# Optimization experiments

Hardware: AMD Instinct MI355X
Metric: run time of the kernel (lower is better)

Reference implementation:

```python
import jax, jax.numpy as jnp
import numpy as np

K_NEIGHBORS = 8

def _cdist(x, y):
    x2 = jnp.sum(x * x, axis=-1)[:, None]
    y2 = jnp.sum(y * y, axis=-1)[None, :]
    d2 = x2 + y2 - 2.0 * (x @ y.T)
    return jnp.sqrt(jnp.maximum(d2, 0.0))

def setup_inputs() -> dict:
    key = jax.random.key(0)
    ks = jax.random.split(key, 16)
    B, C, H, W = 8, 384, 64, 64
    s = lambda fan: 1.0 / np.sqrt(fan)
    inp = {
        'fea': jax.random.normal(ks[0], (B, C, H, W), dtype=jnp.float32),
        # GCNConv weights (applied as x @ W) and post-aggregation biases
        'W1': jax.random.normal(ks[1], (C, C), jnp.float32) * s(C),
        'b1': jnp.zeros((C,), jnp.float32),
        'W2': jax.random.normal(ks[2], (C, C), jnp.float32) * s(C),
        'b2': jnp.zeros((C,), jnp.float32),
        'W3': jax.random.normal(ks[3], (C, C), jnp.float32) * s(C),
        'b3': jnp.zeros((C,), jnp.float32),
        # uncertainty MLP: C -> C/2 -> C/4 -> 1
        'U1': jax.random.normal(ks[4], (C, C // 2), jnp.float32) * s(C),
        'ub1': jnp.zeros((C // 2,), jnp.float32),
        'U2': jax.random.normal(ks[5], (C // 2, C // 4), jnp.float32) * s(C // 2),
        'ub2': jnp.zeros((C // 4,), jnp.float32),
        'U3': jax.random.normal(ks[6], (C // 4, 1), jnp.float32) * s(C // 4),
        'ub3': jnp.zeros((1,), jnp.float32),
    }
    return inp

def _build_graph(fea, k):
    B, C, H, W = fea.shape
    N = H * W
    gy, gx = jnp.meshgrid(jnp.arange(H), jnp.arange(W), indexing='ij')
    coord = jnp.stack([gy, gx], axis=-1).astype(jnp.float32).reshape(N, 2)
    fea_mean = fea.reshape(B, C, N).transpose(0, 2, 1).mean(0)  # [N, C]
    spatial_dist = _cdist(coord, coord)
    feature_dist = _cdist(fea_mean, fea_mean)
    combined = 0.7 * spatial_dist + 0.3 * feature_dist
    _, topk_idx = jax.lax.top_k(-combined, k)  # smallest-k per row
    src = jnp.repeat(jnp.arange(N), k)         # edge_index[0]
    dst = topk_idx.reshape(-1)                 # edge_index[1]
    return src, dst, N

def _gcn_conv(x, W, b, src, dst, N):
    # PyG GCNConv with symmetric normalization; self-loops are guaranteed
    # by construction (diag of combined dist is 0, strictly minimal), so
    # add_remaining_self_loops is a no-op.
    xw = x @ W                                              # [B, N, C]
    deg = jnp.zeros((N,), x.dtype).at[dst].add(1.0)
    dinv = jax.lax.rsqrt(deg)
    norm = dinv[src] * dinv[dst]                            # [E]
    msgs = xw[:, src, :] * norm[None, :, None]              # [B, E, C]
    out = jnp.zeros_like(xw).at[:, dst, :].add(msgs)
    return out + b

def reference(fea, W1, b1, W2, b2, W3, b3, U1, ub1, U2, ub2, U3, ub3):
    B, C, H, W = fea.shape
    src, dst, N = _build_graph(fea, K_NEIGHBORS)
    x = fea.reshape(B, C, N).transpose(0, 2, 1)             # [B, N, C]
    x = x + jax.nn.relu(_gcn_conv(x, W1, b1, src, dst, N))
    x = x + jax.nn.relu(_gcn_conv(x, W2, b2, src, dst, N))
    x = x + jax.nn.relu(_gcn_conv(x, W3, b3, src, dst, N))
    h = jax.nn.gelu(x @ U1 + ub1)
    h = jax.nn.gelu(h @ U2 + ub2)
    unc = jax.nn.sigmoid(h @ U3 + ub3)                      # [B, N, 1]
    unc = unc.reshape(B, 1, H, W)
    return fea * (1.0 + unc)
```

## Files before the change

kernel.cpp:

```cpp
#include <hip/hip_runtime.h>
#include <hip/hip_bf16.h>
#include <math.h>

#define N_NODES 4096
#define C_DIM   384
#define B_DIM   8
#define K_NB    8
#define E_TOT   (N_NODES * K_NB)
#define M_ROWS  (B_DIM * N_NODES)
#define NCHUNK  4
#define SROW    40

typedef unsigned long long u64;
typedef unsigned short u16;
typedef __attribute__((ext_vector_type(8))) short bf16x8;
typedef __attribute__((ext_vector_type(4))) float f32x4;
#define KEY_INF 0xFFFFFFFFFFFFFFFFull

__device__ __forceinline__ u16 f2bf(float f) {
  unsigned u = __float_as_uint(f);
  u += 0x7FFFu + ((u >> 16) & 1u);
  return (u16)(u >> 16);
}
__device__ __forceinline__ float bf2f(u16 h) {
  return __uint_as_float((unsigned)h << 16);
}
__device__ __forceinline__ f32x4 mfma16(bf16x8 a, bf16x8 b, f32x4 c) {
  return __builtin_amdgcn_mfma_f32_16x16x32_bf16(a, b, c, 0, 0, 0);
}
__device__ __forceinline__ void gl_lds16(const u16* gp, u16* lp) {
  __builtin_amdgcn_global_load_lds(
      (const __attribute__((address_space(1))) unsigned int*)gp,
      (__attribute__((address_space(3))) unsigned int*)lp, 16, 0, 0);
}
__device__ __forceinline__ int xcd_swz(int bid, int nwg) {
  return (bid & 7) * (nwg >> 3) + (bid >> 3);
}

__device__ __forceinline__ void ce(u64& a, u64& b) {
  u64 lo = a < b ? a : b;
  u64 hi = a < b ? b : a;
  a = lo; b = hi;
}
__device__ __forceinline__ void ins8(u64 key, u64 (&r)[8]) {
  if (key < r[7]) {
    #pragma unroll
    for (int i = 0; i < 8; i++) {
      u64 lo = key < r[i] ? key : r[i];
      u64 hi = key < r[i] ? r[i] : key;
      r[i] = lo; key = hi;
    }
  }
}
__device__ __forceinline__ void merge8(u64 (&r)[8], const u64 (&o)[8]) {
  u64 c[8];
  #pragma unroll
  for (int i = 0; i < 8; i++) c[i] = r[i] < o[7 - i] ? r[i] : o[7 - i];
  ce(c[0], c[4]); ce(c[1], c[5]); ce(c[2], c[6]); ce(c[3], c[7]);
  ce(c[0], c[2]); ce(c[1], c[3]); ce(c[4], c[6]); ce(c[5], c[7]);
  ce(c[0], c[1]); ce(c[2], c[3]); ce(c[4], c[5]); ce(c[6], c[7]);
  #pragma unroll
  for (int i = 0; i < 8; i++) r[i] = c[i];
}

__global__ __launch_bounds__(256) void k_prep_w(
    const float* __restrict__ W1, const float* __restrict__ W2,
    const float* __restrict__ W3, const float* __restrict__ U1,
    const float* __restrict__ U2,
    u16* __restrict__ Wt1, u16* __restrict__ Wt2, u16* __restrict__ Wt3,
    u16* __restrict__ U1t, u16* __restrict__ U2t) {
  int idx = blockIdx.x * 256 + threadIdx.x;
  if (idx < 147456) {
    int n = idx / 384, k = idx % 384;
    Wt1[idx] = f2bf(W1[k * 384 + n]);
  } else if (idx < 294912) {
    int i = idx - 147456; int n = i / 384, k = i % 384;
    Wt2[i] = f2bf(W2[k * 384 + n]);
  } else if (idx < 442368) {
    int i = idx - 294912; int n = i / 384, k = i % 384;
    Wt3[i] = f2bf(W3[k * 384 + n]);
  } else if (idx < 516096) {
    int i = idx - 442368; int n = i / 384, k = i % 384;
    U1t[i] = f2bf(U1[k * 192 + n]);
  } else if (idx < 534528) {
    int i = idx - 516096; int n = i / 192, k = i % 192;
    U2t[i] = f2bf(U2[k * 96 + n]);
  }
}

__global__ __launch_bounds__(256) void k_transpose_mean(
    const float* __restrict__ fea, u16* __restrict__ Xb,
    u16* __restrict__ fh, u16* __restrict__ fl) {
  __shared__ float tb[32][132];
  __shared__ float ac[32][132];
  int n0 = blockIdx.x * 128, c0 = blockIdx.y * 32;
  int tx = threadIdx.x, ty = threadIdx.y;
  int flat = ty * 32 + tx;
  int g = flat & 3;
  int r2 = flat >> 2;
  for (int i = ty; i < 32; i += 8) {
    #pragma unroll
    for (int e = 0; e < 4; e++) ac[i][tx * 4 + e] = 0.0f;
  }
  __syncthreads();
  for (int b = 0; b < B_DIM; b++) {
    for (int i = ty; i < 32; i += 8) {
      float4 v = *(const float4*)(fea +
          ((size_t)b * C_DIM + (c0 + i)) * N_NODES + n0 + tx * 4);
      *(float4*)&tb[i][tx * 4] = v;
      ac[i][tx * 4 + 0] += v.x;
      ac[i][tx * 4 + 1] += v.y;
      ac[i][tx * 4 + 2] += v.z;
      ac[i][tx * 4 + 3] += v.w;
    }
    __syncthreads();
    #pragma unroll
    for (int half = 0; half < 2; half++) {
      int r = r2 + 64 * half;
      bf16x8 v;
      #pragma unroll
      for (int cc = 0; cc < 8; cc++) v[cc] = (short)f2bf(tb[g * 8 + cc][r]);
      *(bf16x8*)&Xb[((size_t)b * N_NODES + n0 + r) * C_DIM + c0 + g * 8] = v;
    }
    __syncthreads();
  }
  #pragma unroll
  for (int half = 0; half < 2; half++) {
    int r = r2 + 64 * half;
    bf16x8 vh, vl;
    #pragma unroll
    for (int cc = 0; cc < 8; cc++) {
      float m = ac[g * 8 + cc][r] * 0.125f;
      u16 h = f2bf(m);
      vh[cc] = (short)h;
      vl[cc] = (short)f2bf(m - bf2f(h));
    }
    size_t o = (size_t)(n0 + r) * C_DIM + c0 + g * 8;
    *(bf16x8*)&fh[o] = vh;
    *(bf16x8*)&fl[o] = vl;
  }
}

__global__ __launch_bounds__(64) void k_x2(const u16* __restrict__ fh,
                                           const u16* __restrict__ fl,
                                           float* __restrict__ x2) {
  int n = blockIdx.x;
  int lane = threadIdx.x;
  const u16* rh = fh + (size_t)n * C_DIM;
  const u16* rl = fl + (size_t)n * C_DIM;
  float s = 0.0f;
  for (int c = lane; c < C_DIM; c += 64) {
    float v = bf2f(rh[c]) + bf2f(rl[c]);
    s += v * v;
  }
  for (int d = 32; d > 0; d >>= 1) s += __shfl_down(s, d);
  if (lane == 0) x2[n] = s;
}

__global__ __launch_bounds__(256) void k_dist_win(
    const u16* __restrict__ fh, const u16* __restrict__ fl,
    const float* __restrict__ x2, u64* __restrict__ pk,
    int* __restrict__ deg, int* __restrict__ cnt) {
  __shared__ u16 WH[400 * SROW];
  __shared__ u16 WL[400 * SROW];
  int t = threadIdx.x;
  int lane = t & 63, w = t >> 6;
  int p = blockIdx.x;
  int py = p >> 4, px = p & 15;
  int iy0 = py * 4, ix0 = px * 4;
  int l15 = lane & 15;
  int kb = (lane >> 4) * 8;

  if (p < 16) { deg[p * 256 + t] = 0; cnt[p * 256 + t] = 0; }

  int t0 = (w == 0) ? 0 : 7 + (w - 1) * 6;
  int nt = w ? 6 : 7;

  int jj[7]; float x2j[7]; int jy_[7], jx_[7];
  #pragma unroll
  for (int tt = 0; tt < 7; tt++) {
    int s = (t0 + tt) * 16 + l15;
    int sy = s / 20, sx = s - sy * 20;
    int jy = iy0 - 8 + sy, jx = ix0 - 8 + sx;
    bool v = (tt < nt) && ((unsigned)jy < 64u) && ((unsigned)jx < 64u);
    jj[tt] = v ? (jy * 64 + jx) : -1;
    jy_[tt] = jy; jx_[tt] = jx;
    x2j[tt] = v ? x2[jy * 64 + jx] : 0.0f;
  }
  int pr = 168 + (l15 >> 2) * 20 + (l15 & 3);

  int seg = t & 3;
  int rb = t >> 2;

  f32x4 acc[7];
  #pragma unroll
  for (int tt = 0; tt < 7; tt++) acc[tt] = (f32x4){0.f, 0.f, 0.f, 0.f};

  for (int kc = 0; kc < 12; kc++) {
    int k0 = kc * 32;
    __syncthreads();
    #pragma unroll
    for (int it = 0; it < 7; it++) {
      int r = rb + 64 * it;
      if (r < 400) {
        int sy = r / 20, sx = r - sy * 20;
        int jy = iy0 - 8 + sy, jx = ix0 - 8 + sx;
        int j = (((unsigned)jy < 64u) && ((unsigned)jx < 64u)) ? jy * 64 + jx : 0;
        size_t src = (size_t)j * C_DIM + k0 + seg * 8;
        *(bf16x8*)&WH[r * SROW + seg * 8] = *(const bf16x8*)(fh + src);
        *(bf16x8*)&WL[r * SROW + seg * 8] = *(const bf16x8*)(fl + src);
      }
    }
    __syncthreads();
    bf16x8 aH = *(const bf16x8*)&WH[pr * SROW + kb];
    bf16x8 aL = *(const bf16x8*)&WL[pr * SROW + kb];
    #pragma unroll
    for (int tt = 0; tt < 7; tt++) {
      int row = (t0 + tt) * 16 + l15;
      bf16x8 bH = *(const bf16x8*)&WH[row * SROW + kb];
      bf16x8 bL = *(const bf16x8*)&WL[row * SROW + kb];
      acc[tt] = mfma16(aH, bH, acc[tt]);
      acc[tt] = mfma16(aL, bH, acc[tt]);
      acc[tt] = mfma16(aH, bL, acc[tt]);
    }
  }

  #pragma unroll
  for (int r = 0; r < 4; r++) {
    int r16 = ((lane >> 4) << 2) + r;
    int iy = iy0 + (r16 >> 2), ix = ix0 + (r16 & 3);
    int i = iy * 64 + ix;
    float x2i = x2[i];
    u64 top[8];
    #pragma unroll
    for (int q = 0; q < 8; q++) top[q] = KEY_INF;
    #pragma unroll
    for (int tt = 0; tt < 7; tt++) {
      float d2 = x2i + x2j[tt] - 2.0f * acc[tt][r];
      float fd = sqrtf(fmaxf(d2, 0.0f));
      float dy = (float)(iy - jy_[tt]), dx = (float)(ix - jx_[tt]);
      float sd = sqrtf(dy * dy + dx * dx);
      float comb = 0.7f * sd + 0.3f * fd;
      u64 key = (jj[tt] >= 0)
                    ? (((u64)__float_as_uint(comb) << 12) | (u64)jj[tt])
                    : KEY_INF;
      ins8(key, top);
    }
    #pragma unroll
    for (int d = 1; d < 16; d <<= 1) {
      u64 o[8];
      #pragma unroll
      for (int q = 0; q < 8; q++) o[q] = __shfl_xor(top[q], d);
      merge8(top, o);
    }
    if (l15 == 0) {
      #pragma unroll
      for (int q = 0; q < 8; q++)
        pk[((size_t)w * N_NODES + i) * 8 + q] = top[q];
    }
  }
}

__global__ __launch_bounds__(256) void k_topk_merge_fb(
    const u64* __restrict__ pk, const u16* __restrict__ fh,
    const u16* __restrict__ fl, const float* __restrict__ x2,
    int* __restrict__ tk, int* __restrict__ deg) {
  __shared__ int fl_list[256];
  __shared__ int fl_cnt;
  int t = threadIdx.x;
  if (t == 0) fl_cnt = 0;
  __syncthreads();
  int n = blockIdx.x * 256 + t;
  {
    u64 r[8];
    #pragma unroll
    for (int q = 0; q < 8; q++) r[q] = KEY_INF;
    for (int c = 0; c < NCHUNK; c++) {
      const u64* lst = pk + ((size_t)c * N_NODES + n) * 8;
      #pragma unroll
      for (int q = 0; q < 8; q++) {
        u64 key = lst[q];
        if (key >= r[7]) break;
        ins8(key, r);
      }
    }
    float c8 = __uint_as_float((unsigned)(r[7] >> 12));
    if (c8 > 6.28f) {
      int pos = atomicAdd(&fl_cnt, 1);
      fl_list[pos] = n;
    } else {
      #pragma unroll
      for (int o = 0; o < 8; o++) {
        int idx = (int)(r[o] & 0xFFF);
        tk[n * 8 + o] = idx;
        atomicAdd(&deg[idx], 1);
      }
    }
  }
  __syncthreads();
  int nf = fl_cnt;
  int w = t >> 6, lane = t & 63;
  for (int fi = w; fi < nf; fi += 4) {
    int nn = fl_list[fi];
    u64 top[8];
    #pragma unroll
    for (int q = 0; q < 8; q++) top[q] = KEY_INF;
    float x2i = x2[nn];
    int iy = nn >> 6, ix = nn & 63;
    const u16* rh = fh + (size_t)nn * C_DIM;
    const u16* rl = fl + (size_t)nn * C_DIM;
    for (int jb = 0; jb < N_NODES; jb += 64) {
      int j = jb + lane;
      const u16* ch = fh + (size_t)j * C_DIM;
      const u16* cl = fl + (size_t)j * C_DIM;
      float dot = 0.0f;
      for (int k2 = 0; k2 < C_DIM; k2++)
        dot += (bf2f(rh[k2]) + bf2f(rl[k2])) * (bf2f(ch[k2]) + bf2f(cl[k2]));
      float d2 = x2i + x2[j] - 2.0f * dot;
      float fd = sqrtf(fmaxf(d2, 0.0f));
      float dy = (float)(iy - (j >> 6)), dx = (float)(ix - (j & 63));
      float sd = sqrtf(dy * dy + dx * dx);
      float comb = 0.7f * sd + 0.3f * fd;
      ins8(((u64)__float_as_uint(comb) << 12) | (u64)j, top);
    }
    #pragma unroll
    for (int d = 1; d < 64; d <<= 1) {
      u64 o[8];
      #pragma unroll
      for (int q = 0; q < 8; q++) o[q] = __shfl_xor(top[q], d);
      merge8(top, o);
    }
    if (lane == 0) {
      #pragma unroll
      for (int q = 0; q < 8; q++) {
        int idx = (int)(top[q] & 0xFFF);
        tk[nn * 8 + q] = idx;
        atomicAdd(&deg[idx], 1);
      }
    }
  }
}

__global__ __launch_bounds__(256) void k_scan(const int* __restrict__ deg,
                                              int* __restrict__ offs,
                                              float* __restrict__ dinv) {
  __shared__ int ps[256];
  int t = threadIdx.x;
  int base = t * 16;
  int loc[16]; int s = 0;
  for (int i = 0; i < 16; i++) { int d = deg[base + i]; loc[i] = s; s += d; }
  ps[t] = s;
  __syncthreads();
  for (int d = 1; d < 256; d <<= 1) {
    int add = (t >= d) ? ps[t - d] : 0;
    __syncthreads();
    ps[t] += add;
    __syncthreads();
  }
  int cbase = (t == 0) ? 0 : ps[t - 1];
  for (int i = 0; i < 16; i++) offs[base + i] = cbase + loc[i];
  if (t == 255) offs[N_NODES] = ps[255];
  for (int i = 0; i < 16; i++)
    dinv[base + i] = 1.0f / sqrtf((float)deg[base + i]);
}

__global__ __launch_bounds__(256) void k_fill(const int* __restrict__ tk,
                                              const int* __restrict__ offs,
                                              int* __restrict__ cnt,
                                              int* __restrict__ insrc) {
  int e = blockIdx.x * 256 + threadIdx.x;
  if (e >= E_TOT) return;
  int i = e >> 3;
  int n = tk[e];
  int pos = offs[n] + atomicAdd(&cnt[n], 1);
  insrc[pos] = i;
}

__global__ __launch_bounds__(256) void k_sort(const int* __restrict__ offs,
                                              int* __restrict__ insrc) {
  int n = blockIdx.x * 256 + threadIdx.x;
  if (n >= N_NODES) return;
  int beg = offs[n], end = offs[n + 1];
  for (int a = beg + 1; a < end; a++) {
    int v = insrc[a]; int p = a;
    while (p > beg && insrc[p - 1] > v) { insrc[p] = insrc[p - 1]; p--; }
    insrc[p] = v;
  }
}

__device__ __forceinline__ float gelu_f(float x) {
  const float k0 = 0.7978845608028654f;
  float x3 = x * x * x;
  return 0.5f * x * (1.0f + tanhf(k0 * (x + 0.044715f * x3)));
}

template <int EPI>
__global__ __launch_bounds__(256) void k_gemm_lds(
    const u16* __restrict__ A, const u16* __restrict__ Bt,
    const float* __restrict__ bias, u16* __restrict__ Cout,
    int M, int N, int K, int nnt) {
  __shared__ u16 As[2 * 128 * 32];
  __shared__ u16 Bs[2 * 128 * 32];
  const int BO = 128 * 32;
  int wg = xcd_swz(blockIdx.x, gridDim.x);
  int mt = wg / nnt, ntile = wg - mt * nnt;
  int m0 = mt * 128;
  int n0 = ntile * 128;
  int t = threadIdx.x, lane = t & 63, w = t >> 6;
  int l15 = lane & 15;
  int kg = lane >> 4;
  int wr = (w >> 1) * 64, wc = (w & 1) * 64;

  int srow = w * 32 + (lane >> 2);
  int scol = (lane & 3) * 8;
  const u16* gA0 = A + (size_t)(m0 + srow) * K + scol;
  const u16* gA1 = A + (size_t)(m0 + srow + 16) * K + scol;
  int br0 = n0 + srow;      br0 = (br0 < N) ? br0 : 0;
  int br1 = n0 + srow + 16; br1 = (br1 < N) ? br1 : 0;
  const u16* gB0 = Bt + (size_t)br0 * K + scol;
  const u16* gB1 = Bt + (size_t)br1 * K + scol;
  int lo0 = (w * 32) * 32;
  int lo1 = (w * 32 + 16) * 32;

  f32x4 acc[4][4];
  #pragma unroll
  for (int s = 0; s < 4; s++)
    #pragma unroll
    for (int nt = 0; nt < 4; nt++) acc[s][nt] = (f32x4){0.f, 0.f, 0.f, 0.f};

  gl_lds16(gA0, &As[lo0]);
  gl_lds16(gA1, &As[lo1]);
  gl_lds16(gB0, &Bs[lo0]);
  gl_lds16(gB1, &Bs[lo1]);
  __syncthreads();

  int NT = K / 32;
  for (int kt = 0; kt < NT; kt++) {
    int cur = (kt & 1) * BO;
    if (kt + 1 < NT) {
      int nb = ((kt + 1) & 1) * BO;
      int ko = (kt + 1) * 32;
      gl_lds16(gA0 + ko, &As[nb + lo0]);
      gl_lds16(gA1 + ko, &As[nb + lo1]);
      gl_lds16(gB0 + ko, &Bs[nb + lo0]);
      gl_lds16(gB1 + ko, &Bs[nb + lo1]);
    }
    bf16x8 a[4], b[4];
    #pragma unroll
    for (int s = 0; s < 4; s++)
      a[s] = *(const bf16x8*)&As[cur + (wr + s * 16 + l15) * 32 + kg * 8];
    #pragma unroll
    for (int nt = 0; nt < 4; nt++)
      b[nt] = *(const bf16x8*)&Bs[cur + (wc + nt * 16 + l15) * 32 + kg * 8];
    #pragma unroll
    for (int s = 0; s < 4; s++)
      #pragma unroll
      for (int nt = 0; nt < 4; nt++)
        acc[s][nt] = mfma16(a[s], b[nt], acc[s][nt]);
    if (kt + 1 < NT) __syncthreads();
  }

  #pragma unroll
  for (int s = 0; s < 4; s++) {
    int rbase = m0 + wr + s * 16 + ((lane >> 4) << 2);
    #pragma unroll
    for (int nt = 0; nt < 4; nt++) {
      int n = n0 + wc + nt * 16 + l15;
      if (n >= N) continue;
      float bb = (EPI == 1) ? bias[n] : 0.0f;
      #pragma unroll
      for (int r = 0; r < 4; r++) {
        int m = rbase + r;
        float v = acc[s][nt][r];
        if (EPI == 1) { v += bb; v = gelu_f(v); }
        Cout[(size_t)m * N + n] = f2bf(v);
      }
    }
  }
}

__global__ __launch_bounds__(256) void k_mlp2(
    const u16* __restrict__ A, const u16* __restrict__ Bt,
    const float* __restrict__ ub2, const float* __restrict__ U3,
    const float* __restrict__ ub3, float* __restrict__ unc) {
  const int K = 192;
  int t = threadIdx.x, lane = t & 63, w = t >> 6;
  int m0 = blockIdx.x * 128 + w * 32;
  int l15 = lane & 15;
  int kb = (lane >> 4) * 8;

  f32x4 acc[2][6];
  #pragma unroll
  for (int s = 0; s < 2; s++)
    #pragma unroll
    for (int nt = 0; nt < 6; nt++) acc[s][nt] = (f32x4){0.f, 0.f, 0.f, 0.f};

  const u16* ap = A + (size_t)(m0 + l15) * K + kb;
  const u16* bp[6];
  #pragma unroll
  for (int nt = 0; nt < 6; nt++)
    bp[nt] = Bt + (size_t)(nt * 16 + l15) * K + kb;
  const size_t RA = (size_t)16 * K;

  #pragma unroll
  for (int kk = 0; kk < K; kk += 32) {
    bf16x8 a[2], b[6];
    #pragma unroll
    for (int s = 0; s < 2; s++) a[s] = *(const bf16x8*)(ap + s * RA + kk);
    #pragma unroll
    for (int nt = 0; nt < 6; nt++) b[nt] = *(const bf16x8*)(bp[nt] + kk);
    #pragma unroll
    for (int s = 0; s < 2; s++)
      #pragma unroll
      for (int nt = 0; nt < 6; nt++)
        acc[s][nt] = mfma16(a[s], b[nt], acc[s][nt]);
  }

  float ub3v = ub3[0];
  float u3v[6], b2v[6];
  #pragma unroll
  for (int nt = 0; nt < 6; nt++) {
    int col = nt * 16 + l15;
    u3v[nt] = U3[col];
    b2v[nt] = ub2[col];
  }
  #pragma unroll
  for (int s = 0; s < 2; s++) {
    #pragma unroll
    for (int r = 0; r < 4; r++) {
      float part = 0.0f;
      #pragma unroll
      for (int nt = 0; nt < 6; nt++)
        part += gelu_f(acc[s][nt][r] + b2v[nt]) * u3v[nt];
      #pragma unroll
      for (int d = 1; d < 16; d <<= 1) part += __shfl_xor(part, d);
      if (l15 == 0) {
        int m = m0 + s * 16 + ((lane >> 4) << 2) + r;
        unc[m] = 1.0f / (1.0f + expf(-(part + ub3v)));
      }
    }
  }
}

__global__ __launch_bounds__(384) void k_gcn_agg(
    const u16* __restrict__ xw, u16* __restrict__ Xb,
    const float* __restrict__ bias, const float* __restrict__ dinv,
    const int* __restrict__ offs, const int* __restrict__ insrc) {
  const size_t PLANE = (size_t)N_NODES * C_DIM;
  int t = threadIdx.x;
  int g = t / 48, l = t % 48;
  int blk = xcd_swz(blockIdx.x, gridDim.x);
  int slot = blk * 8 + g;
  int n = slot >> 1;
  int hb = (slot & 1) * 4;
  int beg = offs[n], end = offs[n + 1];
  int c0 = l * 8;
  const u16* base = xw + c0 + (size_t)hb * PLANE;

  float a0[8] = {}, a1[8] = {}, a2[8] = {}, a3[8] = {};
  for (int e = beg; e < end; e++) {
    int i = insrc[e];
    float dv = dinv[i];
    const u16* rp = base + (size_t)i * C_DIM;
    bf16x8 v0 = *(const bf16x8*)(rp);
    bf16x8 v1 = *(const bf16x8*)(rp + PLANE);
    bf16x8 v2 = *(const bf16x8*)(rp + 2 * PLANE);
    bf16x8 v3 = *(const bf16x8*)(rp + 3 * PLANE);
    #pragma unroll
    for (int ch = 0; ch < 8; ch++) {
      a0[ch] += dv * bf2f((u16)v0[ch]);
      a1[ch] += dv * bf2f((u16)v1[ch]);
      a2[ch] += dv * bf2f((u16)v2[ch]);
      a3[ch] += dv * bf2f((u16)v3[ch]);
    }
  }

  float dn = dinv[n];
  float bv[8];
  #pragma unroll
  for (int ch = 0; ch < 8; ch++) bv[ch] = bias[c0 + ch];
  size_t ob = (size_t)n * C_DIM + c0 + (size_t)hb * PLANE;
  u16* xp0 = Xb + ob;
  u16* xp1 = Xb + ob + PLANE;
  u16* xp2 = Xb + ob + 2 * PLANE;
  u16* xp3 = Xb + ob + 3 * PLANE;
  bf16x8 xo0 = *(const bf16x8*)xp0, xo1 = *(const bf16x8*)xp1;
  bf16x8 xo2 = *(const bf16x8*)xp2, xo3 = *(const bf16x8*)xp3;
  bf16x8 xn0, xn1, xn2, xn3;
  #pragma unroll
  for (int ch = 0; ch < 8; ch++) {
    xn0[ch] = (short)f2bf(bf2f((u16)xo0[ch]) + fmaxf(dn * a0[ch] + bv[ch], 0.f));
    xn1[ch] = (short)f2bf(bf2f((u16)xo1[ch]) + fmaxf(dn * a1[ch] + bv[ch], 0.f));
    xn2[ch] = (short)f2bf(bf2f((u16)xo2[ch]) + fmaxf(dn * a2[ch] + bv[ch], 0.f));
    xn3[ch] = (short)f2bf(bf2f((u16)xo3[ch]) + fmaxf(dn * a3[ch] + bv[ch], 0.f));
  }
  *(bf16x8*)xp0 = xn0;
  *(bf16x8*)xp1 = xn1;
  *(bf16x8*)xp2 = xn2;
  *(bf16x8*)xp3 = xn3;
}

__global__ __launch_bounds__(256) void k_final(
    const float* __restrict__ fea, const float* __restrict__ unc,
    float* __restrict__ out) {
  size_t i4 = (size_t)blockIdx.x * 256 + threadIdx.x;
  size_t idx = i4 * 4;
  if (idx >= (size_t)B_DIM * C_DIM * N_NODES) return;
  int b = (int)(idx / ((size_t)C_DIM * N_NODES));
  int n = (int)(idx & (N_NODES - 1));
  float4 f = *(const float4*)(fea + idx);
  float4 u = *(const float4*)(unc + (size_t)b * N_NODES + n);
  float4 o;
  o.x = f.x * (1.0f + u.x);
  o.y = f.y * (1.0f + u.y);
  o.z = f.z * (1.0f + u.z);
  o.w = f.w * (1.0f + u.w);
  *(float4*)(out + idx) = o;
}

extern "C" void kernel_launch(void* const* d_in, const int* in_sizes, int n_in,
                              void* d_out, int out_size, void* d_ws, size_t ws_size,
                              hipStream_t stream) {
  const float* fea = (const float*)d_in[0];
  const float* W1  = (const float*)d_in[1];
  const float* b1  = (const float*)d_in[2];
  const float* W2  = (const float*)d_in[3];
  const float* b2  = (const float*)d_in[4];
  const float* W3  = (const float*)d_in[5];
  const float* b3  = (const float*)d_in[6];
  const float* U1  = (const float*)d_in[7];
  const float* ub1 = (const float*)d_in[8];
  const float* U2  = (const float*)d_in[9];
  const float* ub2 = (const float*)d_in[10];
  const float* U3  = (const float*)d_in[11];
  const float* ub3 = (const float*)d_in[12];
  float* out = (float*)d_out;

  char* ws = (char*)d_ws;
  u16*   Xb   = (u16*)  (ws + 0);
  u16*   XWb  = (u16*)  (ws + 25165824);
  u64*   pk   = (u64*)  (ws + 25165824);
  u16*   h1b  = (u16*)  (ws + 25165824);
  u16*   fh   = (u16*)  (ws + 50331648);
  u16*   fl   = (u16*)  (ws + 53477376);
  float* x2   = (float*)(ws + 56623104);
  int*   tk   = (int*)  (ws + 56639488);
  int*   deg  = (int*)  (ws + 56770560);
  float* dinv = (float*)(ws + 56786944);
  int*   offs = (int*)  (ws + 56803328);
  int*   cnt  = (int*)  (ws + 56820224);
  int*   insrc= (int*)  (ws + 56836608);
  float* unc  = (float*)(ws + 56967680);
  u16*   Wt1  = (u16*)  (ws + 57098752);
  u16*   Wt2  = (u16*)  (ws + 57393664);
  u16*   Wt3  = (u16*)  (ws + 57688576);
  u16*   U1t  = (u16*)  (ws + 57983488);
  u16*   U2t  = (u16*)  (ws + 58130944);

  k_prep_w<<<2088, 256, 0, stream>>>(W1, W2, W3, U1, U2, Wt1, Wt2, Wt3, U1t, U2t);
  k_transpose_mean<<<dim3(N_NODES / 128, C_DIM / 32), dim3(32, 8), 0, stream>>>(
      fea, Xb, fh, fl);
  k_x2<<<N_NODES, 64, 0, stream>>>(fh, fl, x2);
  k_dist_win<<<256, 256, 0, stream>>>(fh, fl, x2, pk, deg, cnt);
  k_topk_merge_fb<<<N_NODES / 256, 256, 0, stream>>>(pk, fh, fl, x2, tk, deg);
  k_scan<<<1, 256, 0, stream>>>(deg, offs, dinv);
  k_fill<<<E_TOT / 256, 256, 0, stream>>>(tk, offs, cnt, insrc);
  k_sort<<<N_NODES / 256, 256, 0, stream>>>(offs, insrc);
  const u16* Wl[3] = {Wt1, Wt2, Wt3};
  const float* bl[3] = {b1, b2, b3};
  for (int l = 0; l < 3; l++) {
    k_gemm_lds<3><<<(M_ROWS / 128) * 3, 256, 0, stream>>>(
        Xb, Wl[l], nullptr, XWb, M_ROWS, C_DIM, C_DIM, 3);
    k_gcn_agg<<<N_NODES / 4, 384, 0, stream>>>(XWb, Xb, bl[l], dinv, offs, insrc);
  }
  k_gemm_lds<1><<<(M_ROWS / 128) * 2, 256, 0, stream>>>(
      Xb, U1t, ub1, h1b, M_ROWS, 192, C_DIM, 2);
  k_mlp2<<<M_ROWS / 128, 256, 0, stream>>>(h1b, U2t, ub2, U3, ub3, unc);
  size_t tot = (size_t)B_DIM * C_DIM * N_NODES;
  k_final<<<(tot / 4 + 255) / 256, 256, 0, stream>>>(fea, unc, out);
}
```

Baseline: 270.6 us.

## Fuse prep kernels, spread top-k merge over more blocks, unroll GCN gather

Merges the weight-prep and transpose/mean kernels into one launch so the two independent jobs run side by side, removing one launch. The top-k merge kernel now has each block handle 64 nodes with 256 threads, giving 64 blocks instead of 16 so the small serial merge uses more CUs. The GCN aggregation loop is unrolled by two edges so more gather loads are in flight at once. The cost is more register pressure in the aggregation and idle threads in the merge blocks.

```diff
diff --git a/kernel.cpp b/kernel.cpp
--- a/kernel.cpp
+++ b/kernel.cpp
@@ -63,81 +63,81 @@
   for (int i = 0; i < 8; i++) r[i] = c[i];
 }
 
-__global__ __launch_bounds__(256) void k_prep_w(
+__global__ __launch_bounds__(256) void k_prep_all(
+    const float* __restrict__ fea,
     const float* __restrict__ W1, const float* __restrict__ W2,
     const float* __restrict__ W3, const float* __restrict__ U1,
     const float* __restrict__ U2,
+    u16* __restrict__ Xb, u16* __restrict__ fh, u16* __restrict__ fl,
     u16* __restrict__ Wt1, u16* __restrict__ Wt2, u16* __restrict__ Wt3,
     u16* __restrict__ U1t, u16* __restrict__ U2t) {
-  int idx = blockIdx.x * 256 + threadIdx.x;
-  if (idx < 147456) {
-    int n = idx / 384, k = idx % 384;
-    Wt1[idx] = f2bf(W1[k * 384 + n]);
-  } else if (idx < 294912) {
-    int i = idx - 147456; int n = i / 384, k = i % 384;
-    Wt2[i] = f2bf(W2[k * 384 + n]);
-  } else if (idx < 442368) {
-    int i = idx - 294912; int n = i / 384, k = i % 384;
-    Wt3[i] = f2bf(W3[k * 384 + n]);
-  } else if (idx < 516096) {
-    int i = idx - 442368; int n = i / 384, k = i % 384;
-    U1t[i] = f2bf(U1[k * 192 + n]);
-  } else if (idx < 534528) {
-    int i = idx - 516096; int n = i / 192, k = i % 192;
-    U2t[i] = f2bf(U2[k * 96 + n]);
-  }
-}
-
-__global__ __launch_bounds__(256) void k_transpose_mean(
-    const float* __restrict__ fea, u16* __restrict__ Xb,
-    u16* __restrict__ fh, u16* __restrict__ fl) {
   __shared__ float tb[32][132];
   __shared__ float ac[32][132];
-  int n0 = blockIdx.x * 128, c0 = blockIdx.y * 32;
-  int tx = threadIdx.x, ty = threadIdx.y;
-  int flat = ty * 32 + tx;
-  int g = flat & 3;
-  int r2 = flat >> 2;
-  for (int i = ty; i < 32; i += 8) {
-    #pragma unroll
-    for (int e = 0; e < 4; e++) ac[i][tx * 4 + e] = 0.0f;
-  }
-  __syncthreads();
-  for (int b = 0; b < B_DIM; b++) {
+  int blk = blockIdx.x;
+  int t = threadIdx.x;
+  if (blk < 384) {
+    int n0 = (blk & 31) * 128, c0 = (blk >> 5) * 32;
+    int tx = t & 31, ty = t >> 5;
+    int g = t & 3, r2 = t >> 2;
     for (int i = ty; i < 32; i += 8) {
-      float4 v = *(const float4*)(fea +
-          ((size_t)b * C_DIM + (c0 + i)) * N_NODES + n0 + tx * 4);
-      *(float4*)&tb[i][tx * 4] = v;
-      ac[i][tx * 4 + 0] += v.x;
-      ac[i][tx * 4 + 1] += v.y;
-      ac[i][tx * 4 + 2] += v.z;
-      ac[i][tx * 4 + 3] += v.w;
+      #pragma unroll
+      for (int e = 0; e < 4; e++) ac[i][tx * 4 + e] = 0.0f;
     }
     __syncthreads();
+    for (int b = 0; b < B_DIM; b++) {
+      for (int i = ty; i < 32; i += 8) {
+        float4 v = *(const float4*)(fea +
+            ((size_t)b * C_DIM + (c0 + i)) * N_NODES + n0 + tx * 4);
+        *(float4*)&tb[i][tx * 4] = v;
+        ac[i][tx * 4 + 0] += v.x;
+        ac[i][tx * 4 + 1] += v.y;
+        ac[i][tx * 4 + 2] += v.z;
+        ac[i][tx * 4 + 3] += v.w;
+      }
+      __syncthreads();
+      #pragma unroll
+      for (int half = 0; half < 2; half++) {
+        int r = r2 + 64 * half;
+        bf16x8 v;
+        #pragma unroll
+        for (int cc = 0; cc < 8; cc++) v[cc] = (short)f2bf(tb[g * 8 + cc][r]);
+        *(bf16x8*)&Xb[((size_t)b * N_NODES + n0 + r) * C_DIM + c0 + g * 8] = v;
+      }
+      __syncthreads();
+    }
     #pragma unroll
     for (int half = 0; half < 2; half++) {
       int r = r2 + 64 * half;
-      bf16x8 v;
-      #pragma unroll
-      for (int cc = 0; cc < 8; cc++) v[cc] = (short)f2bf(tb[g * 8 + cc][r]);
-      *(bf16x8*)&Xb[((size_t)b * N_NODES + n0 + r) * C_DIM + c0 + g * 8] = v;
-    }
-    __syncthreads();
-  }
-  #pragma unroll
-  for (int half = 0; half < 2; half++) {
-    int r = r2 + 64 * half;
-    bf16x8 vh, vl;
-    #pragma unroll
-    for (int cc = 0; cc < 8; cc++) {
-      float m = ac[g * 8 + cc][r] * 0.125f;
-      u16 h = f2bf(m);
-      vh[cc] = (short)h;
-      vl[cc] = (short)f2bf(m - bf2f(h));
-    }
-    size_t o = (size_t)(n0 + r) * C_DIM + c0 + g * 8;
-    *(bf16x8*)&fh[o] = vh;
-    *(bf16x8*)&fl[o] = vl;
+      bf16x8 vh, vl;
+      #pragma unroll
+      for (int cc = 0; cc < 8; cc++) {
+        float m = ac[g * 8 + cc][r] * 0.125f;
+        u16 h = f2bf(m);
+        vh[cc] = (short)h;
+        vl[cc] = (short)f2bf(m - bf2f(h));
+      }
+      size_t o = (size_t)(n0 + r) * C_DIM + c0 + g * 8;
+      *(bf16x8*)&fh[o] = vh;
+      *(bf16x8*)&fl[o] = vl;
+    }
+  } else {
+    int idx = (blk - 384) * 256 + t;
+    if (idx < 147456) {
+      int n = idx / 384, k = idx % 384;
+      Wt1[idx] = f2bf(W1[k * 384 + n]);
+    } else if (idx < 294912) {
+      int i = idx - 147456; int n = i / 384, k = i % 384;
+      Wt2[i] = f2bf(W2[k * 384 + n]);
+    } else if (idx < 442368) {
+      int i = idx - 294912; int n = i / 384, k = i % 384;
+      Wt3[i] = f2bf(W3[k * 384 + n]);
+    } else if (idx < 516096) {
+      int i = idx - 442368; int n = i / 384, k = i % 384;
+      U1t[i] = f2bf(U1[k * 192 + n]);
+    } else if (idx < 534528) {
+      int i = idx - 516096; int n = i / 192, k = i % 192;
+      U2t[i] = f2bf(U2[k * 96 + n]);
+    }
   }
 }
 
@@ -265,13 +265,13 @@
     const u64* __restrict__ pk, const u16* __restrict__ fh,
     const u16* __restrict__ fl, const float* __restrict__ x2,
     int* __restrict__ tk, int* __restrict__ deg) {
-  __shared__ int fl_list[256];
+  __shared__ int fl_list[64];
   __shared__ int fl_cnt;
   int t = threadIdx.x;
   if (t == 0) fl_cnt = 0;
   __syncthreads();
-  int n = blockIdx.x * 256 + t;
-  {
+  if (t < 64) {
+    int n = blockIdx.x * 64 + t;
     u64 r[8];
     #pragma unroll
     for (int q = 0; q < 8; q++) r[q] = KEY_INF;
@@ -558,7 +558,36 @@
   const u16* base = xw + c0 + (size_t)hb * PLANE;
 
   float a0[8] = {}, a1[8] = {}, a2[8] = {}, a3[8] = {};
-  for (int e = beg; e < end; e++) {
+  int e = beg;
+  for (; e + 1 < end; e += 2) {
+    int i0 = insrc[e], i1 = insrc[e + 1];
+    float dv0 = dinv[i0], dv1 = dinv[i1];
+    const u16* rp0 = base + (size_t)i0 * C_DIM;
+    const u16* rp1 = base + (size_t)i1 * C_DIM;
+    bf16x8 u0 = *(const bf16x8*)(rp0);
+    bf16x8 u1 = *(const bf16x8*)(rp0 + PLANE);
+    bf16x8 u2 = *(const bf16x8*)(rp0 + 2 * PLANE);
+    bf16x8 u3 = *(const bf16x8*)(rp0 + 3 * PLANE);
+    bf16x8 v0 = *(const bf16x8*)(rp1);
+    bf16x8 v1 = *(const bf16x8*)(rp1 + PLANE);
+    bf16x8 v2 = *(const bf16x8*)(rp1 + 2 * PLANE);
+    bf16x8 v3 = *(const bf16x8*)(rp1 + 3 * PLANE);
+    #pragma unroll
+    for (int ch = 0; ch < 8; ch++) {
+      a0[ch] += dv0 * bf2f((u16)u0[ch]);
+      a1[ch] += dv0 * bf2f((u16)u1[ch]);
+      a2[ch] += dv0 * bf2f((u16)u2[ch]);
+      a3[ch] += dv0 * bf2f((u16)u3[ch]);
+    }
+    #pragma unroll
+    for (int ch = 0; ch < 8; ch++) {
+      a0[ch] += dv1 * bf2f((u16)v0[ch]);
+      a1[ch] += dv1 * bf2f((u16)v1[ch]);
+      a2[ch] += dv1 * bf2f((u16)v2[ch]);
+      a3[ch] += dv1 * bf2f((u16)v3[ch]);
+    }
+  }
+  if (e < end) {
     int i = insrc[e];
     float dv = dinv[i];
     const u16* rp = base + (size_t)i * C_DIM;
@@ -657,12 +686,11 @@
   u16*   U1t  = (u16*)  (ws + 57983488);
   u16*   U2t  = (u16*)  (ws + 58130944);
 
-  k_prep_w<<<2088, 256, 0, stream>>>(W1, W2, W3, U1, U2, Wt1, Wt2, Wt3, U1t, U2t);
-  k_transpose_mean<<<dim3(N_NODES / 128, C_DIM / 32), dim3(32, 8), 0, stream>>>(
-      fea, Xb, fh, fl);
+  k_prep_all<<<384 + 2088, 256, 0, stream>>>(
+      fea, W1, W2, W3, U1, U2, Xb, fh, fl, Wt1, Wt2, Wt3, U1t, U2t);
   k_x2<<<N_NODES, 64, 0, stream>>>(fh, fl, x2);
   k_dist_win<<<256, 256, 0, stream>>>(fh, fl, x2, pk, deg, cnt);
-  k_topk_merge_fb<<<N_NODES / 256, 256, 0, stream>>>(pk, fh, fl, x2, tk, deg);
+  k_topk_merge_fb<<<N_NODES / 64, 256, 0, stream>>>(pk, fh, fl, x2, tk, deg);
   k_scan<<<1, 256, 0, stream>>>(deg, offs, dinv);
   k_fill<<<E_TOT / 256, 256, 0, stream>>>(tk, offs, cnt, insrc);
   k_sort<<<N_NODES / 256, 256, 0, stream>>>(offs, insrc);
```

Result: no change. 275.8 us (+1.9%).
